# Kernel tuning notes

Hardware: AMD Instinct MI355X
Metric: run time of the kernel (lower is better)

The kernel has to match this reference:

```python
import jax, jax.numpy as jnp
import numpy as np

N = 50000          # total nodes across batched graphs
E = 800000         # directed edges (before self-loops)
F_IN = 6           # node_features
HID = 64           # hidden_dim
H = 4              # GAT heads
NG = 1024          # number of graphs in batch
GRID_SIZE = 5      # efficient-kan defaults
SPLINE_K = 3
NEG_SLOPE = 0.2    # GATConv LeakyReLU slope


def setup_inputs() -> dict:
    key = jax.random.key(0)
    ks = jax.random.split(key, 20)
    s = 0.1
    d1 = H * HID  # 256
    inp = {
        "x": jax.random.normal(ks[0], (N, F_IN), dtype=jnp.float32),
        "edge_index": jax.random.randint(ks[1], (2, E), 0, N, dtype=jnp.int64),
        "batch": jnp.sort(jax.random.randint(ks[2], (N,), 0, NG, dtype=jnp.int64)),
        "W1": jax.random.normal(ks[3], (F_IN, d1)) * s,
        "a_src1": jax.random.normal(ks[4], (H, HID)) * s,
        "a_dst1": jax.random.normal(ks[5], (H, HID)) * s,
        "b1": jnp.zeros((d1,), jnp.float32),
        "W2": jax.random.normal(ks[6], (d1, d1)) * s,
        "a_src2": jax.random.normal(ks[7], (H, HID)) * s,
        "a_dst2": jax.random.normal(ks[8], (H, HID)) * s,
        "b2": jnp.zeros((d1,), jnp.float32),
        # KAN layer 1: 256 -> 32
        "base_w1": jax.random.normal(ks[9], (32, d1)) * s,
        "spline_w1": jax.random.normal(ks[10], (32, d1, GRID_SIZE + SPLINE_K)) * s,
        "scaler1": jax.random.normal(ks[11], (32, d1)) * s + 1.0,
        # KAN layer 2: 32 -> 1
        "base_w2": jax.random.normal(ks[12], (1, 32)) * s,
        "spline_w2": jax.random.normal(ks[13], (1, 32, GRID_SIZE + SPLINE_K)) * s,
        "scaler2": jax.random.normal(ks[14], (1, 32)) * s + 1.0,
    }
    return inp


def _gat_conv(x, edge_index, W, a_src, a_dst, bias):
    """PyG GATConv (concat=True, eval mode, self-loops added)."""
    n = x.shape[0]
    src, dst = edge_index[0], edge_index[1]
    xw = (x @ W).reshape(n, H, HID)                      # [N,H,C]
    alpha_s = jnp.einsum('nhc,hc->nh', xw, a_src)        # [N,H]
    alpha_d = jnp.einsum('nhc,hc->nh', xw, a_dst)
    e = alpha_s[src] + alpha_d[dst]                      # [E,H]
    e = jax.nn.leaky_relu(e, NEG_SLOPE)
    # segment softmax over destination nodes
    m = jax.ops.segment_max(e, dst, num_segments=n)      # [N,H]
    ex = jnp.exp(e - m[dst])
    den = jax.ops.segment_sum(ex, dst, num_segments=n)
    alpha = ex / (den[dst] + 1e-16)                      # [E,H]
    msg = alpha[:, :, None] * xw[src]                    # [E,H,C]
    out = jax.ops.segment_sum(msg, dst, num_segments=n)  # [N,H,C]
    return out.reshape(n, H * HID) + bias


def _b_splines(x, grid):
    # x: [B, in]; grid: 1D extended knot vector
    xe = x[..., None]
    b = ((xe >= grid[:-1]) & (xe < grid[1:])).astype(x.dtype)
    for k in range(1, SPLINE_K + 1):
        b = ((xe - grid[:-(k + 1)]) / (grid[k:-1] - grid[:-(k + 1)]) * b[..., :-1]
             + (grid[k + 1:] - xe) / (grid[k + 1:] - grid[1:-k]) * b[..., 1:])
    return b  # [B, in, GRID_SIZE + SPLINE_K]


_H_STEP = 2.0 / GRID_SIZE
_GRID = (jnp.arange(-SPLINE_K, GRID_SIZE + SPLINE_K + 1, dtype=jnp.float32) * _H_STEP - 1.0)


def _kan_linear(x, base_w, spline_w, scaler):
    spline_out = jnp.einsum('nip,oip->no', _b_splines(x, _GRID), spline_w * scaler[..., None])
    return jax.nn.silu(x) @ base_w.T + spline_out


def reference(x, edge_index, batch, W1, a_src1, a_dst1, b1, W2, a_src2, a_dst2, b2,
              base_w1, spline_w1, scaler1, base_w2, spline_w2, scaler2):
    n = x.shape[0]
    loops = jnp.arange(n, dtype=edge_index.dtype)
    ei = jnp.concatenate([edge_index, jnp.stack([loops, loops])], axis=1)  # add self-loops
    h = jax.nn.elu(_gat_conv(x, ei, W1, a_src1, a_dst1, b1))
    h = jax.nn.elu(_gat_conv(h, ei, W2, a_src2, a_dst2, b2))
    # global mean pool over graphs
    sums = jax.ops.segment_sum(h, batch, num_segments=NG)
    cnt = jax.ops.segment_sum(jnp.ones((n,), h.dtype), batch, num_segments=NG)
    pooled = sums / jnp.maximum(cnt, 1.0)[:, None]       # [NG, 256]
    z = _kan_linear(pooled, base_w1, spline_w1, scaler1)  # [NG, 32]
    return _kan_linear(z, base_w2, spline_w2, scaler2)    # [NG, 1]
```

## Files before the change

kernel.cpp:

```cpp
#include <hip/hip_runtime.h>
#include <math.h>

#define HEADS 4
#define HID 64
#define D1 256
#define NGR 1024
#define NEG 0.2f

typedef __attribute__((ext_vector_type(8))) short bf16x8;
typedef __attribute__((ext_vector_type(4))) float f32x4;

static inline int cdiv(int a, int b) { return (a + b - 1) / b; }

__device__ inline unsigned short f2b(float f) {
    union { float f; unsigned u; } v; v.f = f;
    unsigned r = v.u + 0x7FFFu + ((v.u >> 16) & 1u);
    return (unsigned short)(r >> 16);
}
__device__ inline float b2f(unsigned short u) {
    union { unsigned u; float f; } v; v.u = ((unsigned)u) << 16;
    return v.f;
}


__global__ void k_deg(const int* __restrict__ ei, int E, int ET, int* __restrict__ deg) {
    int e = blockIdx.x * blockDim.x + threadIdx.x;
    if (e >= ET) return;
    int d = (e < E) ? ei[E + e] : e - E;
    atomicAdd(&deg[d], 1);
}

__global__ void k_scan1(const int* __restrict__ deg, int* __restrict__ rowp,
                        int* __restrict__ part, int N) {
    __shared__ int sd[256];
    int t = threadIdx.x;
    int i = blockIdx.x * 256 + t;
    int v = (i < N) ? deg[i] : 0;
    sd[t] = v;
    __syncthreads();
    for (int off = 1; off < 256; off <<= 1) {
        int u = (t >= off) ? sd[t - off] : 0;
        __syncthreads();
        sd[t] += u;
        __syncthreads();
    }
    if (i <= N) rowp[i] = sd[t] - v;
    if (t == 255) part[blockIdx.x] = sd[255];
}

__global__ void k_scan2(int* __restrict__ part, int P) {
    __shared__ int sp[1024];
    int t = threadIdx.x;
    int v = (t < P) ? part[t] : 0;
    sp[t] = v;
    __syncthreads();
    for (int off = 1; off < 1024; off <<= 1) {
        int u = (t >= off) ? sp[t - off] : 0;
        __syncthreads();
        sp[t] += u;
        __syncthreads();
    }
    if (t < P) part[t] = sp[t] - v;
}

__global__ void k_scan3(int* __restrict__ rowp, const int* __restrict__ part, int NP1) {
    int i = blockIdx.x * 256 + threadIdx.x;
    if (i < NP1) rowp[i] += part[blockIdx.x];
}

__global__ void k_scatter(const int* __restrict__ ei, int E, int ET,
                          const int* __restrict__ rowp, int* __restrict__ fill,
                          int* __restrict__ csrc) {
    int e = blockIdx.x * blockDim.x + threadIdx.x;
    if (e >= ET) return;
    int s, d;
    if (e < E) { s = ei[e]; d = ei[E + e]; } else { s = d = e - E; }
    int pos = rowp[d] + atomicAdd(&fill[d], 1);
    csrc[pos] = s;
}

__global__ void k_prep(const float* __restrict__ W1, const float* __restrict__ asrc1,
                       const float* __restrict__ adst1, float* __restrict__ va1) {
    int id = threadIdx.x;
    if (id >= 48) return;
    int k = id / 8, h8 = id % 8;
    int h = h8 & 3;
    const float* avec = (h8 < 4) ? (asrc1 + h * HID) : (adst1 + h * HID);
    const float* wrow = W1 + k * D1 + h * HID;
    float s = 0.f;
#pragma unroll 8
    for (int j = 0; j < HID; ++j) s += wrow[j] * avec[j];
    va1[k * 8 + h8] = s;
}

__global__ void k_cvtW(const float* __restrict__ W, const float* __restrict__ asrc2,
                       const float* __restrict__ adst2, unsigned short* __restrict__ Bt) {
    int c = blockIdx.x, k = threadIdx.x;
    float v;
    if (c < 256) {
        v = W[k * D1 + c];
    } else {
        int h = (c - 256) & 3;
        const float* avec = (c < 260) ? (asrc2 + h * HID) : (adst2 + h * HID);
        const float* wrow = W + k * D1 + h * HID;
        float s = 0.f;
#pragma unroll 8
        for (int j = 0; j < HID; ++j) s += wrow[j] * avec[j];
        v = s;
    }
    Bt[c * D1 + k] = f2b(v);
}

__global__ void k_alpha1(const float* __restrict__ x, const float* __restrict__ va1,
                         float* __restrict__ as_, float* __restrict__ ad_, int N) {
    int n = blockIdx.x * blockDim.x + threadIdx.x;
    if (n >= N) return;
    float2 x01 = *(const float2*)(x + n * 6);
    float2 x23 = *(const float2*)(x + n * 6 + 2);
    float2 x45 = *(const float2*)(x + n * 6 + 4);
    float xv[6] = {x01.x, x01.y, x23.x, x23.y, x45.x, x45.y};
    float4 sv, dv;
#pragma unroll
    for (int h = 0; h < 4; ++h) {
        float s = 0.f, d = 0.f;
#pragma unroll
        for (int k = 0; k < 6; ++k) {
            s += xv[k] * va1[k * 8 + h];
            d += xv[k] * va1[k * 8 + 4 + h];
        }
        (&sv.x)[h] = s; (&dv.x)[h] = d;
    }
    ((float4*)as_)[n] = sv;
    ((float4*)ad_)[n] = dv;
}

__global__ void k_aggr1(const int* __restrict__ rowp, const int* __restrict__ csrc,
                        const float* __restrict__ as_, const float* __restrict__ ad_,
                        const float* __restrict__ x, const float* __restrict__ W1,
                        const float* __restrict__ b1, unsigned short* __restrict__ outb, int N) {
    int d = blockIdx.x * 16 + (threadIdx.x >> 4);
    if (d >= N) return;
    int q = threadIdx.x & 15;
    int h = q >> 2, j = q & 3;
    int lo = rowp[d], hi = rowp[d + 1];
    float adh = ad_[d * HEADS + h];
    float a0 = 0.f, a1 = 0.f, a2 = 0.f, a3 = 0.f, a4 = 0.f, a5 = 0.f;
    float den = 0.f;
    for (int k = lo + j; k < hi; k += 4) {
        int s = csrc[k];
        float v = as_[s * HEADS + h] + adh;
        v = v > 0.f ? v : NEG * v;
        float e = __expf(v);
        den += e;
        float2 x01 = *(const float2*)(x + s * 6);
        float2 x23 = *(const float2*)(x + s * 6 + 2);
        float2 x45 = *(const float2*)(x + s * 6 + 4);
        a0 += e * x01.x; a1 += e * x01.y;
        a2 += e * x23.x; a3 += e * x23.y;
        a4 += e * x45.x; a5 += e * x45.y;
    }
#pragma unroll
    for (int off = 1; off < 4; off <<= 1) {
        den += __shfl_xor(den, off);
        a0 += __shfl_xor(a0, off); a1 += __shfl_xor(a1, off);
        a2 += __shfl_xor(a2, off); a3 += __shfl_xor(a3, off);
        a4 += __shfl_xor(a4, off); a5 += __shfl_xor(a5, off);
    }
    float inv = 1.f / (den + 1e-16f);
    int c0 = q * 16;
    unsigned short ob[16];
#pragma unroll
    for (int cc = 0; cc < 16; ++cc) {
        int c = c0 + cc;
        float o = a0 * W1[c] + a1 * W1[D1 + c] + a2 * W1[2 * D1 + c] +
                  a3 * W1[3 * D1 + c] + a4 * W1[4 * D1 + c] + a5 * W1[5 * D1 + c];
        o = o * inv + b1[c];
        o = o > 0.f ? o : (__expf(o) - 1.f);
        ob[cc] = f2b(o);
    }
#pragma unroll
    for (int v = 0; v < 4; ++v)
        ((ushort4*)(outb + (size_t)d * D1 + c0))[v] =
            make_ushort4(ob[v * 4], ob[v * 4 + 1], ob[v * 4 + 2], ob[v * 4 + 3]);
}

#define BPITCH 264
__global__ void k_mm(const unsigned short* __restrict__ A, const unsigned short* __restrict__ Bt,
                     unsigned short* __restrict__ C, float* __restrict__ as_,
                     float* __restrict__ ad_, int N) {
    __shared__ unsigned short sb[80 * BPITCH];
    int nwg = gridDim.x;
    int bid = blockIdx.x;
    int xcd = bid & 7, off = bid >> 3;
    int qq = nwg >> 3, rr = nwg & 7;
    int lin = (xcd < rr) ? (xcd * (qq + 1) + off) : (rr * (qq + 1) + (xcd - rr) * qq + off);
    int xblk = lin >> 2, y = lin & 3;

    int t = threadIdx.x;
#pragma unroll
    for (int c = 0; c < 10; ++c) {
        int idx = c * 256 + t;
        int r = idx >> 5, ch = idx & 31;
        uint4 v = make_uint4(0, 0, 0, 0);
        int src = -1;
        if (r < 64) src = y * 64 + r;
        else if (r < 72 && y == 0) src = 256 + (r - 64);
        if (src >= 0) v = *(const uint4*)(Bt + (size_t)src * D1 + ch * 8);
        *(uint4*)(&sb[r * BPITCH + ch * 8]) = v;
    }
    __syncthreads();

    int w = t >> 6, l = t & 63;
    int lr = l & 15, lk = (l >> 4) * 8;
    int r0w = xblk * 256 + w * 64;
    const unsigned short* aptr[4];
#pragma unroll
    for (int m = 0; m < 4; ++m) {
        int ar = r0w + m * 16 + lr;
        if (ar >= N) ar = N - 1;
        aptr[m] = A + (size_t)ar * D1 + lk;
    }
    f32x4 acc[4][4];
    f32x4 accE[4];
#pragma unroll
    for (int m = 0; m < 4; ++m) {
        accE[m] = (f32x4){0.f, 0.f, 0.f, 0.f};
#pragma unroll
        for (int n = 0; n < 4; ++n) acc[m][n] = (f32x4){0.f, 0.f, 0.f, 0.f};
    }
#pragma unroll
    for (int ks = 0; ks < 8; ++ks) {
        bf16x8 av[4];
#pragma unroll
        for (int m = 0; m < 4; ++m) av[m] = *(const bf16x8*)(aptr[m] + ks * 32);
#pragma unroll
        for (int n = 0; n < 4; ++n) {
            bf16x8 bv = *(const bf16x8*)(&sb[(n * 16 + lr) * BPITCH + ks * 32 + lk]);
#pragma unroll
            for (int m = 0; m < 4; ++m)
                acc[m][n] = __builtin_amdgcn_mfma_f32_16x16x32_bf16(av[m], bv, acc[m][n], 0, 0, 0);
        }
        if (y == 0) {
            bf16x8 be = *(const bf16x8*)(&sb[(64 + lr) * BPITCH + ks * 32 + lk]);
#pragma unroll
            for (int m = 0; m < 4; ++m)
                accE[m] = __builtin_amdgcn_mfma_f32_16x16x32_bf16(av[m], be, accE[m], 0, 0, 0);
        }
    }
    int rsub = (l >> 4) * 4;
#pragma unroll
    for (int m = 0; m < 4; ++m) {
#pragma unroll
        for (int r = 0; r < 4; ++r) {
            int row = r0w + m * 16 + rsub + r;
            if (row < N) {
#pragma unroll
                for (int n = 0; n < 4; ++n)
                    C[(size_t)row * D1 + y * 64 + n * 16 + lr] = f2b(acc[m][n][r]);
            }
        }
    }
    if (y == 0) {
#pragma unroll
        for (int m = 0; m < 4; ++m) {
#pragma unroll
            for (int r = 0; r < 4; ++r) {
                int row = r0w + m * 16 + rsub + r;
                if (row < N) {
                    float v = accE[m][r];
                    if (lr < 4) as_[row * HEADS + lr] = v;
                    else if (lr < 8) ad_[row * HEADS + (lr - 4)] = v;
                }
            }
        }
    }
}

__global__ void k_aggr2(const int* __restrict__ rowp, const int* __restrict__ csrc,
                        const float* __restrict__ as_, const float* __restrict__ ad_,
                        const unsigned short* __restrict__ xb, const float* __restrict__ bias,
                        unsigned short* __restrict__ outb, int N) {
    int d = blockIdx.x * 4 + (threadIdx.x >> 6);
    if (d >= N) return;
    int t = threadIdx.x & 63;
    int h = t >> 4;
    int lo = rowp[d], hi = rowp[d + 1];
    float adh = ad_[d * HEADS + h];

    float4 acc = {0.f, 0.f, 0.f, 0.f};
    float den = 0.f;
    int k = lo;
    for (; k + 3 < hi; k += 4) {
        int s0 = csrc[k], s1 = csrc[k + 1], s2 = csrc[k + 2], s3 = csrc[k + 3];
        float v0 = as_[s0 * HEADS + h] + adh; v0 = v0 > 0.f ? v0 : NEG * v0;
        float v1 = as_[s1 * HEADS + h] + adh; v1 = v1 > 0.f ? v1 : NEG * v1;
        float v2 = as_[s2 * HEADS + h] + adh; v2 = v2 > 0.f ? v2 : NEG * v2;
        float v3 = as_[s3 * HEADS + h] + adh; v3 = v3 > 0.f ? v3 : NEG * v3;
        float e0 = __expf(v0), e1 = __expf(v1);
        float e2 = __expf(v2), e3 = __expf(v3);
        ushort4 u0 = ((const ushort4*)(xb + (size_t)s0 * D1))[t];
        ushort4 u1 = ((const ushort4*)(xb + (size_t)s1 * D1))[t];
        ushort4 u2 = ((const ushort4*)(xb + (size_t)s2 * D1))[t];
        ushort4 u3 = ((const ushort4*)(xb + (size_t)s3 * D1))[t];
        den += e0 + e1 + e2 + e3;
        acc.x += e0 * b2f(u0.x) + e1 * b2f(u1.x) + e2 * b2f(u2.x) + e3 * b2f(u3.x);
        acc.y += e0 * b2f(u0.y) + e1 * b2f(u1.y) + e2 * b2f(u2.y) + e3 * b2f(u3.y);
        acc.z += e0 * b2f(u0.z) + e1 * b2f(u1.z) + e2 * b2f(u2.z) + e3 * b2f(u3.z);
        acc.w += e0 * b2f(u0.w) + e1 * b2f(u1.w) + e2 * b2f(u2.w) + e3 * b2f(u3.w);
    }
    for (; k < hi; ++k) {
        int s0 = csrc[k];
        float v0 = as_[s0 * HEADS + h] + adh; v0 = v0 > 0.f ? v0 : NEG * v0;
        float e0 = __expf(v0);
        ushort4 u0 = ((const ushort4*)(xb + (size_t)s0 * D1))[t];
        den += e0;
        acc.x += e0 * b2f(u0.x); acc.y += e0 * b2f(u0.y);
        acc.z += e0 * b2f(u0.z); acc.w += e0 * b2f(u0.w);
    }
    float inv = 1.f / (den + 1e-16f);
    float4 bv = ((const float4*)bias)[t];
    float4 o;
    o.x = acc.x * inv + bv.x;
    o.y = acc.y * inv + bv.y;
    o.z = acc.z * inv + bv.z;
    o.w = acc.w * inv + bv.w;
    o.x = o.x > 0.f ? o.x : (__expf(o.x) - 1.f);
    o.y = o.y > 0.f ? o.y : (__expf(o.y) - 1.f);
    o.z = o.z > 0.f ? o.z : (__expf(o.z) - 1.f);
    o.w = o.w > 0.f ? o.w : (__expf(o.w) - 1.f);
    ushort4 ub; ub.x = f2b(o.x); ub.y = f2b(o.y); ub.z = f2b(o.z); ub.w = f2b(o.w);
    ((ushort4*)(outb + (size_t)d * D1))[t] = ub;
}


__device__ inline float knotf(int j) { return (j - 3) * 0.4f - 1.0f; }

__device__ inline void bspl8(float x, float* out) {
    float t[12];
#pragma unroll
    for (int j = 0; j < 12; ++j) t[j] = knotf(j);
    float bb[11];
#pragma unroll
    for (int j = 0; j < 11; ++j) bb[j] = (x >= t[j] && x < t[j + 1]) ? 1.f : 0.f;
#pragma unroll
    for (int k = 1; k <= 3; ++k) {
#pragma unroll
        for (int j = 0; j + k < 11; ++j) {
            float dl = t[j + k] - t[j];
            float dr = t[j + k + 1] - t[j + 1];
            bb[j] = (x - t[j]) / dl * bb[j] + (t[j + k + 1] - x) / dr * bb[j + 1];
        }
    }
#pragma unroll
    for (int p = 0; p < 8; ++p) out[p] = bb[p];
}

__device__ inline float siluf(float x) { return x / (1.f + __expf(-x)); }

__global__ void k_poolkan(const unsigned short* __restrict__ hb2, const int* __restrict__ batch,
                          const float* __restrict__ bw1, const float* __restrict__ sw1,
                          const float* __restrict__ sc1, const float* __restrict__ bw2,
                          const float* __restrict__ sw2, const float* __restrict__ sc2,
                          float* __restrict__ out, int N) {
    __shared__ float sB[D1][9];
    __shared__ float sS[D1];
    __shared__ float sZ[32];
    int g = blockIdx.x;
    int lo = 0, hi = N;
    while (lo < hi) { int m = (lo + hi) >> 1; if (batch[m] < g) lo = m + 1; else hi = m; }
    int lo2 = lo, hi2 = N;
    while (lo2 < hi2) { int m = (lo2 + hi2) >> 1; if (batch[m] < g + 1) lo2 = m + 1; else hi2 = m; }
    int i = threadIdx.x;
    float s = 0.f;
    for (int n = lo; n < lo2; ++n) s += b2f(hb2[(size_t)n * D1 + i]);
    float xi = s / (float)max(lo2 - lo, 1);
    float b[8];
    bspl8(xi, b);
#pragma unroll
    for (int p = 0; p < 8; ++p) sB[i][p] = b[p];
    sS[i] = siluf(xi);
    __syncthreads();
    int wv = i >> 6, l = i & 63;
    for (int oo = 0; oo < 8; ++oo) {
        int o = wv * 8 + oo;
        float part = 0.f;
        for (int ii = l; ii < D1; ii += 64) {
            float sc = sc1[o * D1 + ii];
            float p0 = sS[ii] * bw1[o * D1 + ii];
            const float* sw = sw1 + ((size_t)o * D1 + ii) * 8;
#pragma unroll
            for (int p = 0; p < 8; ++p) p0 += sB[ii][p] * sw[p] * sc;
            part += p0;
        }
#pragma unroll
        for (int off = 32; off >= 1; off >>= 1) part += __shfl_down(part, off);
        if (l == 0) sZ[o] = part;
    }
    __syncthreads();
    if (i < 64) {
        float part = 0.f;
        if (i < 32) {
            float z = sZ[i];
            float b2a[8];
            bspl8(z, b2a);
            part = siluf(z) * bw2[i];
            float sc = sc2[i];
#pragma unroll
            for (int p = 0; p < 8; ++p) part += b2a[p] * sw2[i * 8 + p] * sc;
        }
#pragma unroll
        for (int off = 32; off >= 1; off >>= 1) part += __shfl_down(part, off);
        if (i == 0) out[g] = part;
    }
}

extern "C" void kernel_launch(void* const* d_in, const int* in_sizes, int n_in,
                              void* d_out, int out_size, void* d_ws, size_t ws_size,
                              hipStream_t stream) {
    const float* x      = (const float*)d_in[0];
    const int*   ei     = (const int*)d_in[1];
    const int*   batch  = (const int*)d_in[2];
    const float* W1     = (const float*)d_in[3];
    const float* asrc1  = (const float*)d_in[4];
    const float* adst1  = (const float*)d_in[5];
    const float* b1     = (const float*)d_in[6];
    const float* W2     = (const float*)d_in[7];
    const float* asrc2  = (const float*)d_in[8];
    const float* adst2  = (const float*)d_in[9];
    const float* b2     = (const float*)d_in[10];
    const float* bw1    = (const float*)d_in[11];
    const float* sw1    = (const float*)d_in[12];
    const float* sc1    = (const float*)d_in[13];
    const float* bw2    = (const float*)d_in[14];
    const float* sw2    = (const float*)d_in[15];
    const float* sc2    = (const float*)d_in[16];
    float* outp = (float*)d_out;

    const int N  = in_sizes[0] / 6;
    const int E  = in_sizes[1] / 2;
    const int ET = E + N;

    char* base = (char*)d_ws;
    unsigned short* hb  = (unsigned short*)base; base += (size_t)N * D1 * 2;
    unsigned short* xb  = (unsigned short*)base; base += (size_t)N * D1 * 2;
    unsigned short* hb2 = (unsigned short*)base; base += (size_t)N * D1 * 2;
    float* as_ = (float*)base;                   base += (size_t)N * HEADS * 4;
    float* ad_ = (float*)base;                   base += (size_t)N * HEADS * 4;
    unsigned short* Btb = (unsigned short*)base; base += (size_t)264 * D1 * 2;
    float* va1 = (float*)base;                   base += 48 * 4;
    int* deg  = (int*)base;                      base += (size_t)N * 4;
    int* fill = (int*)base;                      base += (size_t)N * 4;
    int* rowp = (int*)base;                      base += (size_t)(N + 1) * 4;
    int* part = (int*)base;                      base += 1024 * 4;
    int* csrc = (int*)base;                      base += (size_t)ET * 4;

    const int TB = 256;
    int gET = cdiv(ET, TB);
    int gSC = cdiv(N + 1, 256);

    hipMemsetAsync(deg, 0, (size_t)N * sizeof(int), stream);
    hipMemsetAsync(fill, 0, (size_t)N * sizeof(int), stream);
    k_prep<<<1, 64, 0, stream>>>(W1, asrc1, adst1, va1);
    k_deg<<<gET, TB, 0, stream>>>(ei, E, ET, deg);
    k_scan1<<<gSC, 256, 0, stream>>>(deg, rowp, part, N);
    k_scan2<<<1, 1024, 0, stream>>>(part, gSC);
    k_scan3<<<gSC, 256, 0, stream>>>(rowp, part, N + 1);
    k_scatter<<<gET, TB, 0, stream>>>(ei, E, ET, rowp, fill, csrc);
    k_cvtW<<<264, 256, 0, stream>>>(W2, asrc2, adst2, Btb);

    k_alpha1<<<cdiv(N, TB), TB, 0, stream>>>(x, va1, as_, ad_, N);
    k_aggr1<<<cdiv(N, 16), TB, 0, stream>>>(rowp, csrc, as_, ad_, x, W1, b1, hb, N);

    k_mm<<<cdiv(N, 256) * 4, TB, 0, stream>>>(hb, Btb, xb, as_, ad_, N);
    k_aggr2<<<cdiv(N, 4), TB, 0, stream>>>(rowp, csrc, as_, ad_, xb, b2, hb2, N);

    k_poolkan<<<NGR, TB, 0, stream>>>(hb2, batch, bw1, sw1, sc1, bw2, sw2, sc2, outp, N);
}
```

Measured before the change: 286.2 us.

## Fuse setup kernels and replace three-pass scan with atomic-offset CSR build

Merges memsets, weight conversion and attention-vector prep into one init kernel, and folds the alpha1 computation into the degree-count kernel. The three-kernel prefix scan becomes a single kernel in which each block reserves its base offset with an atomicAdd on a global counter. Row ends are then computed as rowp plus degree. This cuts the launch count from about 12 to 8. The rows are no longer ordered by destination node, which is fine since each row is read only through its own start and degree. The aggr1 output-store loop is also restructured.

```diff
diff --git a/kernel.cpp b/kernel.cpp
--- a/kernel.cpp
+++ b/kernel.cpp
@@ -22,17 +22,72 @@
     return v.f;
 }
 
-
-__global__ void k_deg(const int* __restrict__ ei, int E, int ET, int* __restrict__ deg) {
-    int e = blockIdx.x * blockDim.x + threadIdx.x;
-    if (e >= ET) return;
-    int d = (e < E) ? ei[E + e] : e - E;
-    atomicAdd(&deg[d], 1);
-}
-
-__global__ void k_scan1(const int* __restrict__ deg, int* __restrict__ rowp,
-                        int* __restrict__ part, int N) {
+__global__ void k_init(const float* __restrict__ W1, const float* __restrict__ asrc1,
+                       const float* __restrict__ adst1, const float* __restrict__ W2,
+                       const float* __restrict__ asrc2, const float* __restrict__ adst2,
+                       unsigned short* __restrict__ Btb, float* __restrict__ va1,
+                       int* __restrict__ deg, int* __restrict__ fill,
+                       int* __restrict__ gcnt, int N) {
+    int gt = blockIdx.x * 256 + threadIdx.x, gs = gridDim.x * 256;
+    for (int i = gt; i < N; i += gs) { deg[i] = 0; fill[i] = 0; }
+    for (int i = gt; i < 65536; i += gs) {
+        int c = i & 255, k = i >> 8;
+        Btb[c * D1 + k] = f2b(W2[k * D1 + c]);
+    }
+    for (int i = gt; i < 2048; i += gs) {
+        int c = i >> 8, k = i & 255, h = c & 3;
+        const float* avec = ((c < 4) ? asrc2 : adst2) + h * HID;
+        const float* wrow = W2 + k * D1 + h * HID;
+        float s = 0.f;
+#pragma unroll 8
+        for (int j = 0; j < HID; ++j) s += wrow[j] * avec[j];
+        Btb[(256 + c) * D1 + k] = f2b(s);
+    }
+    for (int i = gt; i < 48; i += gs) {
+        int k = i / 8, h8 = i % 8, h = h8 & 3;
+        const float* avec = (h8 < 4) ? (asrc1 + h * HID) : (adst1 + h * HID);
+        const float* wrow = W1 + k * D1 + h * HID;
+        float s = 0.f;
+#pragma unroll 8
+        for (int j = 0; j < HID; ++j) s += wrow[j] * avec[j];
+        va1[k * 8 + h8] = s;
+    }
+    if (gt == 0) *gcnt = 0;
+}
+
+__global__ void k_dega(const int* __restrict__ ei, int E, int ET, int* __restrict__ deg,
+                       const float* __restrict__ x, const float* __restrict__ va1,
+                       float* __restrict__ as_, float* __restrict__ ad_, int N) {
+    int gt = blockIdx.x * 256 + threadIdx.x, gs = gridDim.x * 256;
+    for (int e = gt; e < ET; e += gs) {
+        int d = (e < E) ? ei[E + e] : e - E;
+        atomicAdd(&deg[d], 1);
+    }
+    for (int n = gt; n < N; n += gs) {
+        float2 x01 = *(const float2*)(x + n * 6);
+        float2 x23 = *(const float2*)(x + n * 6 + 2);
+        float2 x45 = *(const float2*)(x + n * 6 + 4);
+        float xv[6] = {x01.x, x01.y, x23.x, x23.y, x45.x, x45.y};
+        float4 sv, dv;
+#pragma unroll
+        for (int h = 0; h < 4; ++h) {
+            float s = 0.f, d = 0.f;
+#pragma unroll
+            for (int k = 0; k < 6; ++k) {
+                s += xv[k] * va1[k * 8 + h];
+                d += xv[k] * va1[k * 8 + 4 + h];
+            }
+            (&sv.x)[h] = s; (&dv.x)[h] = d;
+        }
+        ((float4*)as_)[n] = sv;
+        ((float4*)ad_)[n] = dv;
+    }
+}
+
+__global__ void k_off(const int* __restrict__ deg, int* __restrict__ rowp,
+                      int* __restrict__ gcnt, int N) {
     __shared__ int sd[256];
+    __shared__ int sbase;
     int t = threadIdx.x;
     int i = blockIdx.x * 256 + t;
     int v = (i < N) ? deg[i] : 0;
@@ -44,28 +99,9 @@
         sd[t] += u;
         __syncthreads();
     }
-    if (i <= N) rowp[i] = sd[t] - v;
-    if (t == 255) part[blockIdx.x] = sd[255];
-}
-
-__global__ void k_scan2(int* __restrict__ part, int P) {
-    __shared__ int sp[1024];
-    int t = threadIdx.x;
-    int v = (t < P) ? part[t] : 0;
-    sp[t] = v;
+    if (t == 255) sbase = atomicAdd(gcnt, sd[255]);
     __syncthreads();
-    for (int off = 1; off < 1024; off <<= 1) {
-        int u = (t >= off) ? sp[t - off] : 0;
-        __syncthreads();
-        sp[t] += u;
-        __syncthreads();
-    }
-    if (t < P) part[t] = sp[t] - v;
-}
-
-__global__ void k_scan3(int* __restrict__ rowp, const int* __restrict__ part, int NP1) {
-    int i = blockIdx.x * 256 + threadIdx.x;
-    if (i < NP1) rowp[i] += part[blockIdx.x];
+    if (i < N) rowp[i] = sbase + sd[t] - v;
 }
 
 __global__ void k_scatter(const int* __restrict__ ei, int E, int ET,
@@ -79,62 +115,8 @@
     csrc[pos] = s;
 }
 
-__global__ void k_prep(const float* __restrict__ W1, const float* __restrict__ asrc1,
-                       const float* __restrict__ adst1, float* __restrict__ va1) {
-    int id = threadIdx.x;
-    if (id >= 48) return;
-    int k = id / 8, h8 = id % 8;
-    int h = h8 & 3;
-    const float* avec = (h8 < 4) ? (asrc1 + h * HID) : (adst1 + h * HID);
-    const float* wrow = W1 + k * D1 + h * HID;
-    float s = 0.f;
-#pragma unroll 8
-    for (int j = 0; j < HID; ++j) s += wrow[j] * avec[j];
-    va1[k * 8 + h8] = s;
-}
-
-__global__ void k_cvtW(const float* __restrict__ W, const float* __restrict__ asrc2,
-                       const float* __restrict__ adst2, unsigned short* __restrict__ Bt) {
-    int c = blockIdx.x, k = threadIdx.x;
-    float v;
-    if (c < 256) {
-        v = W[k * D1 + c];
-    } else {
-        int h = (c - 256) & 3;
-        const float* avec = (c < 260) ? (asrc2 + h * HID) : (adst2 + h * HID);
-        const float* wrow = W + k * D1 + h * HID;
-        float s = 0.f;
-#pragma unroll 8
-        for (int j = 0; j < HID; ++j) s += wrow[j] * avec[j];
-        v = s;
-    }
-    Bt[c * D1 + k] = f2b(v);
-}
-
-__global__ void k_alpha1(const float* __restrict__ x, const float* __restrict__ va1,
-                         float* __restrict__ as_, float* __restrict__ ad_, int N) {
-    int n = blockIdx.x * blockDim.x + threadIdx.x;
-    if (n >= N) return;
-    float2 x01 = *(const float2*)(x + n * 6);
-    float2 x23 = *(const float2*)(x + n * 6 + 2);
-    float2 x45 = *(const float2*)(x + n * 6 + 4);
-    float xv[6] = {x01.x, x01.y, x23.x, x23.y, x45.x, x45.y};
-    float4 sv, dv;
-#pragma unroll
-    for (int h = 0; h < 4; ++h) {
-        float s = 0.f, d = 0.f;
-#pragma unroll
-        for (int k = 0; k < 6; ++k) {
-            s += xv[k] * va1[k * 8 + h];
-            d += xv[k] * va1[k * 8 + 4 + h];
-        }
-        (&sv.x)[h] = s; (&dv.x)[h] = d;
-    }
-    ((float4*)as_)[n] = sv;
-    ((float4*)ad_)[n] = dv;
-}
-
-__global__ void k_aggr1(const int* __restrict__ rowp, const int* __restrict__ csrc,
+__global__ void k_aggr1(const int* __restrict__ rowp, const int* __restrict__ deg,
+                        const int* __restrict__ csrc,
                         const float* __restrict__ as_, const float* __restrict__ ad_,
                         const float* __restrict__ x, const float* __restrict__ W1,
                         const float* __restrict__ b1, unsigned short* __restrict__ outb, int N) {
@@ -142,7 +124,7 @@
     if (d >= N) return;
     int q = threadIdx.x & 15;
     int h = q >> 2, j = q & 3;
-    int lo = rowp[d], hi = rowp[d + 1];
+    int lo = rowp[d], hi = lo + deg[d];
     float adh = ad_[d * HEADS + h];
     float a0 = 0.f, a1 = 0.f, a2 = 0.f, a3 = 0.f, a4 = 0.f, a5 = 0.f;
     float den = 0.f;
@@ -168,20 +150,20 @@
     }
     float inv = 1.f / (den + 1e-16f);
     int c0 = q * 16;
-    unsigned short ob[16];
-#pragma unroll
-    for (int cc = 0; cc < 16; ++cc) {
-        int c = c0 + cc;
-        float o = a0 * W1[c] + a1 * W1[D1 + c] + a2 * W1[2 * D1 + c] +
-                  a3 * W1[3 * D1 + c] + a4 * W1[4 * D1 + c] + a5 * W1[5 * D1 + c];
-        o = o * inv + b1[c];
-        o = o > 0.f ? o : (__expf(o) - 1.f);
-        ob[cc] = f2b(o);
-    }
-#pragma unroll
-    for (int v = 0; v < 4; ++v)
-        ((ushort4*)(outb + (size_t)d * D1 + c0))[v] =
-            make_ushort4(ob[v * 4], ob[v * 4 + 1], ob[v * 4 + 2], ob[v * 4 + 3]);
+#pragma unroll
+    for (int v4 = 0; v4 < 4; ++v4) {
+        ushort4 ub;
+#pragma unroll
+        for (int cc = 0; cc < 4; ++cc) {
+            int c = c0 + v4 * 4 + cc;
+            float o = a0 * W1[c] + a1 * W1[D1 + c] + a2 * W1[2 * D1 + c] +
+                      a3 * W1[3 * D1 + c] + a4 * W1[4 * D1 + c] + a5 * W1[5 * D1 + c];
+            o = o * inv + b1[c];
+            o = o > 0.f ? o : (__expf(o) - 1.f);
+            (&ub.x)[cc] = f2b(o);
+        }
+        ((ushort4*)(outb + (size_t)d * D1 + c0))[v4] = ub;
+    }
 }
 
 #define BPITCH 264
@@ -276,7 +258,8 @@
     }
 }
 
-__global__ void k_aggr2(const int* __restrict__ rowp, const int* __restrict__ csrc,
+__global__ void k_aggr2(const int* __restrict__ rowp, const int* __restrict__ deg,
+                        const int* __restrict__ csrc,
                         const float* __restrict__ as_, const float* __restrict__ ad_,
                         const unsigned short* __restrict__ xb, const float* __restrict__ bias,
                         unsigned short* __restrict__ outb, int N) {
@@ -284,7 +267,7 @@
     if (d >= N) return;
     int t = threadIdx.x & 63;
     int h = t >> 4;
-    int lo = rowp[d], hi = rowp[d + 1];
+    int lo = rowp[d], hi = lo + deg[d];
     float adh = ad_[d * HEADS + h];
 
     float4 acc = {0.f, 0.f, 0.f, 0.f};
@@ -333,12 +316,10 @@
 }
 
 
-__device__ inline float knotf(int j) { return (j - 3) * 0.4f - 1.0f; }
-
 __device__ inline void bspl8(float x, float* out) {
     float t[12];
 #pragma unroll
-    for (int j = 0; j < 12; ++j) t[j] = knotf(j);
+    for (int j = 0; j < 12; ++j) t[j] = (j - 3) * 0.4f - 1.0f;
     float bb[11];
 #pragma unroll
     for (int j = 0; j < 11; ++j) bb[j] = (x >= t[j] && x < t[j + 1]) ? 1.f : 0.f;
@@ -451,28 +432,19 @@
     int* deg  = (int*)base;                      base += (size_t)N * 4;
     int* fill = (int*)base;                      base += (size_t)N * 4;
     int* rowp = (int*)base;                      base += (size_t)(N + 1) * 4;
-    int* part = (int*)base;                      base += 1024 * 4;
+    int* gcnt = (int*)base;                      base += 4;
     int* csrc = (int*)base;                      base += (size_t)ET * 4;
 
     const int TB = 256;
     int gET = cdiv(ET, TB);
-    int gSC = cdiv(N + 1, 256);
-
-    hipMemsetAsync(deg, 0, (size_t)N * sizeof(int), stream);
-    hipMemsetAsync(fill, 0, (size_t)N * sizeof(int), stream);
-    k_prep<<<1, 64, 0, stream>>>(W1, asrc1, adst1, va1);
-    k_deg<<<gET, TB, 0, stream>>>(ei, E, ET, deg);
-    k_scan1<<<gSC, 256, 0, stream>>>(deg, rowp, part, N);
-    k_scan2<<<1, 1024, 0, stream>>>(part, gSC);
-    k_scan3<<<gSC, 256, 0, stream>>>(rowp, part, N + 1);
+    int gN  = cdiv(N, TB);
+
+    k_init<<<gN, TB, 0, stream>>>(W1, asrc1, adst1, W2, asrc2, adst2, Btb, va1, deg, fill, gcnt, N);
+    k_dega<<<gET, TB, 0, stream>>>(ei, E, ET, deg, x, va1, as_, ad_, N);
+    k_off<<<gN, TB, 0, stream>>>(deg, rowp, gcnt, N);
     k_scatter<<<gET, TB, 0, stream>>>(ei, E, ET, rowp, fill, csrc);
-    k_cvtW<<<264, 256, 0, stream>>>(W2, asrc2, adst2, Btb);
-
-    k_alpha1<<<cdiv(N, TB), TB, 0, stream>>>(x, va1, as_, ad_, N);
-    k_aggr1<<<cdiv(N, 16), TB, 0, stream>>>(rowp, csrc, as_, ad_, x, W1, b1, hb, N);
-
+    k_aggr1<<<cdiv(N, 16), TB, 0, stream>>>(rowp, deg, csrc, as_, ad_, x, W1, b1, hb, N);
     k_mm<<<cdiv(N, 256) * 4, TB, 0, stream>>>(hb, Btb, xb, as_, ad_, N);
-    k_aggr2<<<cdiv(N, 4), TB, 0, stream>>>(rowp, csrc, as_, ad_, xb, b2, hb2, N);
-
+    k_aggr2<<<cdiv(N, 4), TB, 0, stream>>>(rowp, deg, csrc, as_, ad_, xb, b2, hb2, N);
     k_poolkan<<<NGR, TB, 0, stream>>>(hb2, batch, bw1, sw1, sc1, bw2, sw2, sc2, outp, N);
 }
```

After: 284.5 us. Within noise of the previous version (-0.6%).
